# Kernel tuning notes

Hardware: AMD Instinct MI355X
Metric: run time of the kernel (lower is better)

Reference implementation:

```python
import jax, jax.numpy as jnp
import numpy as np

N_SRC, N_DST, E = 50000, 50000, 800000
D_GT, D_AG = 64, 64
HID, HEADS = 256, 4
FPH = HID // HEADS  # 64
N_ACT = 16
NEG_SLOPE = 0.2  # DGL GATv2Conv default negative_slope


def setup_inputs() -> dict:
    key = jax.random.key(0)
    ks = jax.random.split(key, 16)
    f32 = jnp.float32
    return {
        "feat_gt": jax.random.normal(ks[0], (N_SRC, D_GT), f32),
        "feat_agent": jax.random.normal(ks[1], (N_DST, D_AG), f32),
        "h0": jax.random.normal(ks[2], (N_DST, HID), f32),
        "edge_src": jax.random.randint(ks[3], (E,), 0, N_SRC),
        "edge_dst": jax.random.randint(ks[4], (E,), 0, N_DST),
        "W_src": jax.random.normal(ks[5], (D_GT, HID), f32) * 0.1,
        "b_src": jnp.zeros((HID,), f32),
        "W_dst": jax.random.normal(ks[6], (D_AG, HID), f32) * 0.1,
        "b_dst": jnp.zeros((HID,), f32),
        "attn": jax.random.normal(ks[7], (HEADS, FPH), f32) * 0.1,
        "W_res": jax.random.normal(ks[8], (D_AG, HID), f32) * 0.1,
        "b_res": jnp.zeros((HID,), f32),
        "W_ih": jax.random.normal(ks[9], (3 * HID, HID), f32) * 0.05,
        "W_hh": jax.random.normal(ks[10], (3 * HID, HID), f32) * 0.05,
        "b_ih": jnp.zeros((3 * HID,), f32),
        "b_hh": jnp.zeros((3 * HID,), f32),
        "W_out": jax.random.normal(ks[11], (HID, N_ACT), f32) * 0.05,
        "b_out": jnp.zeros((N_ACT,), f32),
    }


def _gatv2(feat_gt, feat_agent, edge_src, edge_dst,
           W_src, b_src, W_dst, b_dst, attn, W_res, b_res):
    # GATv2Conv (bipartite, share_weights=False, residual=True, activation=ReLU)
    fs = (feat_gt @ W_src + b_src).reshape(N_SRC, HEADS, FPH)    # [Ns,H,F]
    fd = (feat_agent @ W_dst + b_dst).reshape(N_DST, HEADS, FPH)  # [Nd,H,F]
    e = fs[edge_src] + fd[edge_dst]                               # [E,H,F]
    e = jnp.where(e > 0, e, NEG_SLOPE * e)                        # LeakyReLU
    score = jnp.einsum('ehf,hf->eh', e, attn)                     # [E,H]
    # edge softmax segmented by destination node
    smax = jax.lax.stop_gradient(
        jax.ops.segment_max(score, edge_dst, num_segments=N_DST))  # [Nd,H]
    ex = jnp.exp(score - smax[edge_dst])
    den = jax.ops.segment_sum(ex, edge_dst, num_segments=N_DST)   # [Nd,H]
    alpha = ex / den[edge_dst]                                    # [E,H]
    msg = alpha[:, :, None] * fs[edge_src]                        # [E,H,F]
    rst = jax.ops.segment_sum(msg, edge_dst, num_segments=N_DST)  # [Nd,H,F]
    rst = rst.reshape(N_DST, HID) + (feat_agent @ W_res + b_res)  # residual
    return jax.nn.relu(rst)


def _gru_cell(x, h, W_ih, W_hh, b_ih, b_hh):
    gi = x @ W_ih.T + b_ih
    gh = h @ W_hh.T + b_hh
    ir, iz, inn = jnp.split(gi, 3, axis=-1)
    hr, hz, hn = jnp.split(gh, 3, axis=-1)
    r = jax.nn.sigmoid(ir + hr)
    z = jax.nn.sigmoid(iz + hz)
    n = jnp.tanh(inn + r * hn)
    return (1.0 - z) * n + z * h


def reference(feat_gt, feat_agent, h0, edge_src, edge_dst,
              W_src, b_src, W_dst, b_dst, attn, W_res, b_res,
              W_ih, W_hh, b_ih, b_hh, W_out, b_out):
    x = _gatv2(feat_gt, feat_agent, edge_src, edge_dst,
               W_src, b_src, W_dst, b_dst, attn, W_res, b_res)  # [Nd,HID]
    h = _gru_cell(x, h0, W_ih, W_hh, b_ih, b_hh)                # [Nd,HID]
    logits = h @ W_out + b_out                                  # [Nd,N_ACT]
    return (logits, h)
```

## Files before the change

kernel.cpp:

```cpp
#include <hip/hip_runtime.h>
#include <stdint.h>

#define N_SRCN 50000
#define N_DSTN 50000
#define NE     800000
#define HIDN   256
#define NEG    0.2f

typedef __attribute__((ext_vector_type(8)))  short short8;
typedef __attribute__((ext_vector_type(16))) float float16v;

__device__ __forceinline__ float bf2f(unsigned short u){
    union { unsigned u32; float f; } c; c.u32 = ((unsigned)u) << 16; return c.f;
}
__device__ __forceinline__ unsigned short f2bf(float f){
    union { float f; unsigned u; } c; c.f = f;
    unsigned r = c.u + 0x7fffu + ((c.u >> 16) & 1u);
    return (unsigned short)(r >> 16);
}
__device__ __forceinline__ float4 ld4b(const unsigned short* p){
    uint2 u = *reinterpret_cast<const uint2*>(p);
    float4 r;
    r.x = bf2f((unsigned short)(u.x & 0xffff));
    r.y = bf2f((unsigned short)(u.x >> 16));
    r.z = bf2f((unsigned short)(u.y & 0xffff));
    r.w = bf2f((unsigned short)(u.y >> 16));
    return r;
}

__global__ void pack_kernel(const float* __restrict__ Wsrc, const float* __restrict__ Wdst,
                            const float* __restrict__ Wres, const float* __restrict__ Wih,
                            const float* __restrict__ Whh,
                            unsigned short* __restrict__ Wt2,
                            unsigned short* __restrict__ Wf){
    int i = blockIdx.x * 256 + threadIdx.x;
    if (i < 49152){
        int which = i >> 14, j = i & 16383;
        int k = j >> 8, c = j & 255;
        const float* W = (which == 0) ? Wsrc : (which == 1 ? Wdst : Wres);
        float v = W[j];
        int off = which * 16384 + (c >> 5) * 2048 + (k >> 4) * 512
                + (((k >> 3) & 1) * 32 + (c & 31)) * 8 + (k & 7);
        Wt2[off] = f2bf(v);
    } else if (i < 49152 + 196608){
        int o = i - 49152;
        int row = o >> 8, k = o & 255;
        int g = row >> 8, c = row & 255;
        float v = Wih[o];
        int off = g * 131072 + (c >> 5) * 16384 + (k >> 4) * 512
                + (((k >> 3) & 1) * 32 + (c & 31)) * 8 + (k & 7);
        Wf[off] = f2bf(v);
    } else if (i < 49152 + 393216){
        int o = i - 49152 - 196608;
        int row = o >> 8, k = o & 255;
        int g = row >> 8, c = row & 255;
        float v = Whh[o];
        int off = g * 131072 + (c >> 5) * 16384 + (16 + (k >> 4)) * 512
                + (((k >> 3) & 1) * 32 + (c & 31)) * 8 + (k & 7);
        Wf[off] = f2bf(v);
    }
}

__global__ void convh_kernel(const float* __restrict__ h, unsigned short* __restrict__ hb){
    int i = blockIdx.x * 256 + threadIdx.x;
    if (i < N_DSTN * 64){
        float4 v = reinterpret_cast<const float4*>(h)[i];
        uint2 o;
        o.x = (unsigned)f2bf(v.x) | ((unsigned)f2bf(v.y) << 16);
        o.y = (unsigned)f2bf(v.z) | ((unsigned)f2bf(v.w) << 16);
        reinterpret_cast<uint2*>(hb)[i] = o;
    }
}

__global__ __launch_bounds__(256) void proj_kernel(
        const float* __restrict__ A, const unsigned short* __restrict__ Wt2,
        const float* __restrict__ bias, unsigned short* __restrict__ out){
    __shared__ unsigned short As[64 * 72];
    __shared__ unsigned short Cs[64 * 72];
    int tid = threadIdx.x;
    int m0 = blockIdx.y * 64;
    #pragma unroll
    for (int i = 0; i < 4; ++i){
        int ci = tid + i * 256;
        int row = ci >> 4;
        int k4 = (ci & 15) << 2;
        int gr = m0 + row; if (gr >= N_SRCN) gr = N_SRCN - 1;
        float4 v = *reinterpret_cast<const float4*>(A + (size_t)gr * 64 + k4);
        unsigned short* dp = As + row * 72 + k4;
        dp[0] = f2bf(v.x); dp[1] = f2bf(v.y); dp[2] = f2bf(v.z); dp[3] = f2bf(v.w);
    }
    __syncthreads();
    int lane = tid & 63, w = tid >> 6;
    int l31 = lane & 31, half = lane >> 5;
    int msub = (w & 1) * 32;
    int cbw = blockIdx.x * 2 + (w >> 1);
    const unsigned short* bb = Wt2 + cbw * 2048 + lane * 8;
    const unsigned short* ap = As + (msub + l31) * 72 + half * 8;
    float16v acc = {0,0,0,0,0,0,0,0,0,0,0,0,0,0,0,0};
    #pragma unroll
    for (int ks = 0; ks < 4; ++ks){
        short8 a = *reinterpret_cast<const short8*>(ap + ks * 16);
        short8 b = *reinterpret_cast<const short8*>(bb + ks * 512);
        acc = __builtin_amdgcn_mfma_f32_32x32x16_bf16(a, b, acc, 0, 0, 0);
    }
    float bv = bias[cbw * 32 + l31];
    int ccol = (w >> 1) * 32 + l31;
    #pragma unroll
    for (int r = 0; r < 16; ++r){
        int row = (r & 3) + 8 * (r >> 2) + 4 * half + msub;
        Cs[row * 72 + ccol] = f2bf(acc[r] + bv);
    }
    __syncthreads();
    int srow = tid >> 2, chunk = tid & 3;
    int gr2 = m0 + srow;
    if (gr2 < N_SRCN){
        const uint4* sp = reinterpret_cast<const uint4*>(Cs + srow * 72 + chunk * 16);
        uint4* gp = reinterpret_cast<uint4*>(out + (size_t)gr2 * 256 + blockIdx.x * 64 + chunk * 16);
        gp[0] = sp[0];
        gp[1] = sp[1];
    }
}

__global__ void degree_kernel(const int* __restrict__ dst, int* __restrict__ deg){
    int i = blockIdx.x * 256 + threadIdx.x;
    if (i < NE) atomicAdd(&deg[dst[i]], 1);
}

__global__ void scan1_kernel(const int* __restrict__ deg, int* __restrict__ bsum){
    __shared__ int s[256];
    int tid = threadIdx.x;
    int i = blockIdx.x * 256 + tid;
    s[tid] = (i < N_DSTN) ? deg[i] : 0;
    __syncthreads();
    #pragma unroll
    for (int off = 128; off; off >>= 1){
        if (tid < off) s[tid] += s[tid + off];
        __syncthreads();
    }
    if (tid == 0) bsum[blockIdx.x] = s[0];
}

__global__ void scan2_kernel(const int* __restrict__ bsum, int* __restrict__ boff){
    __shared__ int s[256];
    int tid = threadIdx.x;
    int v = (tid < 196) ? bsum[tid] : 0;
    s[tid] = v;
    __syncthreads();
    #pragma unroll
    for (int off = 1; off < 256; off <<= 1){
        int t = (tid >= off) ? s[tid - off] : 0;
        __syncthreads();
        s[tid] += t;
        __syncthreads();
    }
    if (tid < 196) boff[tid] = s[tid] - v;
}

__global__ void scan3_kernel(const int* __restrict__ deg, const int* __restrict__ boff,
                             int* __restrict__ ptr, int* __restrict__ cursor){
    __shared__ int s[256];
    int tid = threadIdx.x;
    int i = blockIdx.x * 256 + tid;
    int v = (i < N_DSTN) ? deg[i] : 0;
    s[tid] = v;
    __syncthreads();
    #pragma unroll
    for (int off = 1; off < 256; off <<= 1){
        int t = (tid >= off) ? s[tid - off] : 0;
        __syncthreads();
        s[tid] += t;
        __syncthreads();
    }
    int ex = s[tid] - v + boff[blockIdx.x];
    if (i < N_DSTN){ ptr[i] = ex; cursor[i] = ex; }
}

__global__ void scatter_kernel(const int* __restrict__ src, const int* __restrict__ dst,
                               int* __restrict__ cursor, int* __restrict__ csr){
    int i = blockIdx.x * 256 + threadIdx.x;
    if (i < NE){
        int d = dst[i];
        int pos = atomicAdd(&cursor[d], 1);
        csr[pos] = src[i];
    }
}

__global__ __launch_bounds__(256) void aggregate_kernel(
        const unsigned short* __restrict__ fs, const unsigned short* __restrict__ fd,
        const unsigned short* __restrict__ res, const float* __restrict__ attn,
        const int* __restrict__ ptr, const int* __restrict__ deg,
        const int* __restrict__ csr, unsigned short* __restrict__ x){
    int wv = threadIdx.x >> 6;
    int d = blockIdx.x * 4 + wv;
    if (d >= N_DSTN) return;
    int lane = threadIdx.x & 63;
    int c4 = lane * 4;
    float4 fdv = ld4b(fd + (size_t)d * 256 + c4);
    float4 at = *reinterpret_cast<const float4*>(attn + (lane >> 4) * 64 + (lane & 15) * 4);
    int p = ptr[d], dg = deg[d];
    float l = 0.f;
    float4 acc = make_float4(0.f, 0.f, 0.f, 0.f);
    for (int base = 0; base < dg; base += 64){
        int cnt = min(64, dg - base);
        int sreg = (lane < cnt) ? csr[p + base + lane] : 0;
        float4 b0 = ld4b(fs + (size_t)__shfl(sreg, 0) * 256 + c4);
        float4 b1 = ld4b(fs + (size_t)__shfl(sreg, 1 & 63) * 256 + c4);
        float4 b2 = ld4b(fs + (size_t)__shfl(sreg, 2 & 63) * 256 + c4);
        float4 b3 = ld4b(fs + (size_t)__shfl(sreg, 3 & 63) * 256 + c4);
        for (int j = 0; j < cnt; j += 4){
            float4 n0 = ld4b(fs + (size_t)__shfl(sreg, (j + 4) & 63) * 256 + c4);
            float4 n1 = ld4b(fs + (size_t)__shfl(sreg, (j + 5) & 63) * 256 + c4);
            float4 n2 = ld4b(fs + (size_t)__shfl(sreg, (j + 6) & 63) * 256 + c4);
            float4 n3 = ld4b(fs + (size_t)__shfl(sreg, (j + 7) & 63) * 256 + c4);
#define PROC(BV, T) { \
            float ex = BV.x + fdv.x; ex = ex > 0.f ? ex : NEG * ex; \
            float ey = BV.y + fdv.y; ey = ey > 0.f ? ey : NEG * ey; \
            float ez = BV.z + fdv.z; ez = ez > 0.f ? ez : NEG * ez; \
            float ew = BV.w + fdv.w; ew = ew > 0.f ? ew : NEG * ew; \
            float part = ex * at.x + ey * at.y + ez * at.z + ew * at.w; \
            part += __shfl_xor(part, 1); \
            part += __shfl_xor(part, 2); \
            part += __shfl_xor(part, 4); \
            part += __shfl_xor(part, 8); \
            float wgt = ((j + (T)) < cnt) ? __expf(part) : 0.f; \
            l += wgt; \
            acc.x = fmaf(wgt, BV.x, acc.x); \
            acc.y = fmaf(wgt, BV.y, acc.y); \
            acc.z = fmaf(wgt, BV.z, acc.z); \
            acc.w = fmaf(wgt, BV.w, acc.w); }
            PROC(b0, 0) PROC(b1, 1) PROC(b2, 2) PROC(b3, 3)
#undef PROC
            b0 = n0; b1 = n1; b2 = n2; b3 = n3;
        }
    }
    float inv = (l > 0.f) ? 1.f / l : 0.f;
    float4 rv = ld4b(res + (size_t)d * 256 + c4);
    float xx = fmaxf(fmaf(acc.x, inv, rv.x), 0.f);
    float xy = fmaxf(fmaf(acc.y, inv, rv.y), 0.f);
    float xz = fmaxf(fmaf(acc.z, inv, rv.z), 0.f);
    float xw = fmaxf(fmaf(acc.w, inv, rv.w), 0.f);
    uint2 o;
    o.x = (unsigned)f2bf(xx) | ((unsigned)f2bf(xy) << 16);
    o.y = (unsigned)f2bf(xz) | ((unsigned)f2bf(xw) << 16);
    *reinterpret_cast<uint2*>(x + (size_t)d * 256 + c4) = o;
}

__global__ __launch_bounds__(256, 3) void gru_kernel(
        const unsigned short* __restrict__ Xb, const unsigned short* __restrict__ Hb,
        const float* __restrict__ H0, const unsigned short* __restrict__ Wf,
        const float* __restrict__ bih, const float* __restrict__ bhh,
        float* __restrict__ outH){
    __shared__ unsigned short As[128 * 136];
    int tid = threadIdx.x;
    int m0 = blockIdx.y * 128;
    int w = tid >> 6, lane = tid & 63;
    int l31 = lane & 31, half = lane >> 5;
    int cb = blockIdx.x;
    int cg = cb * 32 + l31;
    const unsigned short* bb = Wf + cb * 16384 + lane * 8;
    float16v ar  = {0,0,0,0,0,0,0,0,0,0,0,0,0,0,0,0};
    float16v az = ar, anx = ar, anh = ar;
    #pragma unroll
    for (int kc = 0; kc < 512; kc += 128){
        const unsigned short* srcb = (kc < 256) ? (Xb + kc) : (Hb + (kc - 256));
        __syncthreads();
        #pragma unroll
        for (int i = 0; i < 8; ++i){
            int ci = tid + i * 256;
            int row = ci >> 4;
            int k8 = (ci & 15) << 3;
            int gr = m0 + row; if (gr >= N_DSTN) gr = N_DSTN - 1;
            *reinterpret_cast<uint4*>(As + row * 136 + k8) =
                *reinterpret_cast<const uint4*>(srcb + (size_t)gr * 256 + k8);
        }
        __syncthreads();
        const unsigned short* ap = As + (w * 32 + l31) * 136 + half * 8;
        #pragma unroll
        for (int ks = 0; ks < 8; ++ks){
            int kk = (kc >> 4) + ks;
            short8 a  = *reinterpret_cast<const short8*>(ap + ks * 16);
            short8 br = *reinterpret_cast<const short8*>(bb + (size_t)kk * 512);
            short8 bz = *reinterpret_cast<const short8*>(bb + 131072 + (size_t)kk * 512);
            short8 bn = *reinterpret_cast<const short8*>(bb + 262144 + (size_t)kk * 512);
            ar = __builtin_amdgcn_mfma_f32_32x32x16_bf16(a, br, ar, 0, 0, 0);
            az = __builtin_amdgcn_mfma_f32_32x32x16_bf16(a, bz, az, 0, 0, 0);
            if (kc < 256) anx = __builtin_amdgcn_mfma_f32_32x32x16_bf16(a, bn, anx, 0, 0, 0);
            else          anh = __builtin_amdgcn_mfma_f32_32x32x16_bf16(a, bn, anh, 0, 0, 0);
        }
    }
    float rb = bih[cg] + bhh[cg];
    float zb = bih[256 + cg] + bhh[256 + cg];
    float bin = bih[512 + cg], bhn = bhh[512 + cg];
    #pragma unroll
    for (int r = 0; r < 16; ++r){
        int m = m0 + w * 32 + (r & 3) + 8 * (r >> 2) + 4 * half;
        if (m < N_DSTN){
            float h0v = H0[(size_t)m * 256 + cg];
            float rr = 1.f / (1.f + __expf(-(ar[r] + rb)));
            float zz = 1.f / (1.f + __expf(-(az[r] + zb)));
            float nx = anx[r] + bin + rr * (anh[r] + bhn);
            float tm = __expf(-2.f * fabsf(nx));
            float nn = (1.f - tm) / (1.f + tm);
            nn = (nx >= 0.f) ? nn : -nn;
            outH[(size_t)m * 256 + cg] = (1.f - zz) * nn + zz * h0v;
        }
    }
}

__global__ __launch_bounds__(256) void logits_kernel(
        const float* __restrict__ H, const float* __restrict__ Wout,
        const float* __restrict__ bout, float* __restrict__ outL){
    __shared__ float Hl[16 * 260];
    __shared__ float Wl[16 * 260];
    int tid = threadIdx.x;
    int m0 = blockIdx.x * 16;
    #pragma unroll
    for (int i = 0; i < 4; ++i){
        int ci = tid + i * 256;
        int row = ci >> 6;
        int c4 = (ci & 63) << 2;
        int gr = m0 + row; if (gr >= N_DSTN) gr = N_DSTN - 1;
        float4 v = *reinterpret_cast<const float4*>(H + (size_t)gr * 256 + c4);
        float* dp = Hl + row * 260 + c4;
        dp[0] = v.x; dp[1] = v.y; dp[2] = v.z; dp[3] = v.w;
    }
    #pragma unroll
    for (int i = 0; i < 16; ++i){
        int ci = tid + i * 256;
        int c = ci >> 4, j = ci & 15;
        Wl[j * 260 + c] = Wout[c * 16 + j];
    }
    __syncthreads();
    int row = tid >> 4, j = tid & 15;
    const float* hr = Hl + row * 260;
    const float* wr = Wl + j * 260;
    float acc = bout[j];
    #pragma unroll
    for (int c = 0; c < 256; c += 4){
        float4 hv = *reinterpret_cast<const float4*>(hr + c);
        float4 wv = *reinterpret_cast<const float4*>(wr + c);
        acc = fmaf(hv.x, wv.x, fmaf(hv.y, wv.y, fmaf(hv.z, wv.z, fmaf(hv.w, wv.w, acc))));
    }
    int m = m0 + row;
    if (m < N_DSTN) outL[m * 16 + j] = acc;
}

extern "C" void kernel_launch(void* const* d_in, const int* in_sizes, int n_in,
                              void* d_out, int out_size, void* d_ws, size_t ws_size,
                              hipStream_t stream){
    const float* feat_gt = (const float*)d_in[0];
    const float* feat_ag = (const float*)d_in[1];
    const float* h0      = (const float*)d_in[2];
    const int*   e_src   = (const int*)d_in[3];
    const int*   e_dst   = (const int*)d_in[4];
    const float* W_src   = (const float*)d_in[5];
    const float* b_src   = (const float*)d_in[6];
    const float* W_dst   = (const float*)d_in[7];
    const float* b_dst   = (const float*)d_in[8];
    const float* attn    = (const float*)d_in[9];
    const float* W_res   = (const float*)d_in[10];
    const float* b_res   = (const float*)d_in[11];
    const float* W_ih    = (const float*)d_in[12];
    const float* W_hh    = (const float*)d_in[13];
    const float* b_ih    = (const float*)d_in[14];
    const float* b_hh    = (const float*)d_in[15];
    const float* W_out   = (const float*)d_in[16];
    const float* b_out   = (const float*)d_in[17];

    float* outL = (float*)d_out;
    float* outH = outL + (size_t)N_DSTN * 16;

    char* ws = (char*)d_ws;
    size_t off = 0;
    auto alloc = [&](size_t bytes) -> void* {
        void* p = ws + off; off = (off + bytes + 255) & ~(size_t)255; return p;
    };
    unsigned short* fs   = (unsigned short*)alloc((size_t)N_SRCN * 256 * 2);
    unsigned short* fd   = (unsigned short*)alloc((size_t)N_DSTN * 256 * 2);
    unsigned short* res  = (unsigned short*)alloc((size_t)N_DSTN * 256 * 2);
    unsigned short* xb   = (unsigned short*)alloc((size_t)N_DSTN * 256 * 2);
    unsigned short* hb   = (unsigned short*)alloc((size_t)N_DSTN * 256 * 2);
    unsigned short* Wt2  = (unsigned short*)alloc(49152 * 2);
    unsigned short* Wf   = (unsigned short*)alloc(393216 * 2);
    int* deg    = (int*)alloc(N_DSTN * 4);
    int* ptr    = (int*)alloc(N_DSTN * 4);
    int* cursor = (int*)alloc(N_DSTN * 4);
    int* csr    = (int*)alloc((size_t)NE * 4);
    int* bsum   = (int*)alloc(256 * 4);
    int* boff   = (int*)alloc(256 * 4);

    hipMemsetAsync(deg, 0, N_DSTN * 4, stream);
    pack_kernel<<<1728, 256, 0, stream>>>(W_src, W_dst, W_res, W_ih, W_hh, Wt2, Wf);
    convh_kernel<<<12500, 256, 0, stream>>>(h0, hb);

    dim3 pg(4, 782);
    proj_kernel<<<pg, 256, 0, stream>>>(feat_gt, Wt2, b_src, fs);
    proj_kernel<<<pg, 256, 0, stream>>>(feat_ag, Wt2 + 16384, b_dst, fd);
    proj_kernel<<<pg, 256, 0, stream>>>(feat_ag, Wt2 + 32768, b_res, res);

    degree_kernel<<<3125, 256, 0, stream>>>(e_dst, deg);
    scan1_kernel<<<196, 256, 0, stream>>>(deg, bsum);
    scan2_kernel<<<1, 256, 0, stream>>>(bsum, boff);
    scan3_kernel<<<196, 256, 0, stream>>>(deg, boff, ptr, cursor);
    scatter_kernel<<<3125, 256, 0, stream>>>(e_src, e_dst, cursor, csr);
    aggregate_kernel<<<12500, 256, 0, stream>>>(fs, fd, res, attn, ptr, deg, csr, xb);

    gru_kernel<<<dim3(8, 391), 256, 0, stream>>>(xb, hb, h0, Wf, b_ih, b_hh, outH);
    logits_kernel<<<3125, 256, 0, stream>>>(outH, W_out, b_out, outL);
}
```

Before: 497.1 us.

## Fuse h0 bf16 conversion into GRU, merge projection launches, XCD-aware GRU mapping

Removes the separate h0-to-bf16 conversion kernel and its buffer: the GRU kernel now loads fp32 h0 directly and converts it while staging into shared memory. The three projection GEMM launches are merged into one launch using blockIdx.z to select input, weights, bias and output. The GRU grid is flattened and remapped so the 8 column blocks of a row strip land on the same XCD, aiming for L2 reuse of the activation rows, and the occupancy hint is raised from 3 to 4. The tradeoff is that each GRU block now reads fp32 h0, twice the bytes of bf16, for every column block, and the higher occupancy hint may constrain registers.

After: 485.2 us. 2.4% less time.

```diff
diff --git a/kernel.cpp b/kernel.cpp
--- a/kernel.cpp
+++ b/kernel.cpp
@@ -61,22 +61,20 @@
     }
 }
 
-__global__ void convh_kernel(const float* __restrict__ h, unsigned short* __restrict__ hb){
-    int i = blockIdx.x * 256 + threadIdx.x;
-    if (i < N_DSTN * 64){
-        float4 v = reinterpret_cast<const float4*>(h)[i];
-        uint2 o;
-        o.x = (unsigned)f2bf(v.x) | ((unsigned)f2bf(v.y) << 16);
-        o.y = (unsigned)f2bf(v.z) | ((unsigned)f2bf(v.w) << 16);
-        reinterpret_cast<uint2*>(hb)[i] = o;
-    }
-}
-
 __global__ __launch_bounds__(256) void proj_kernel(
-        const float* __restrict__ A, const unsigned short* __restrict__ Wt2,
-        const float* __restrict__ bias, unsigned short* __restrict__ out){
+        const float* __restrict__ Agt, const float* __restrict__ Aag,
+        const unsigned short* __restrict__ Wt2,
+        const float* __restrict__ bsrc, const float* __restrict__ bdst,
+        const float* __restrict__ bres,
+        unsigned short* __restrict__ fs, unsigned short* __restrict__ fd,
+        unsigned short* __restrict__ resb){
     __shared__ unsigned short As[64 * 72];
     __shared__ unsigned short Cs[64 * 72];
+    int z = blockIdx.z;
+    const float* A = (z == 0) ? Agt : Aag;
+    const float* bias = (z == 0) ? bsrc : (z == 1 ? bdst : bres);
+    unsigned short* out = (z == 0) ? fs : (z == 1 ? fd : resb);
+    const unsigned short* Wb = Wt2 + z * 16384;
     int tid = threadIdx.x;
     int m0 = blockIdx.y * 64;
     #pragma unroll
@@ -94,7 +92,7 @@
     int l31 = lane & 31, half = lane >> 5;
     int msub = (w & 1) * 32;
     int cbw = blockIdx.x * 2 + (w >> 1);
-    const unsigned short* bb = Wt2 + cbw * 2048 + lane * 8;
+    const unsigned short* bb = Wb + cbw * 2048 + lane * 8;
     const unsigned short* ap = As + (msub + l31) * 72 + half * 8;
     float16v acc = {0,0,0,0,0,0,0,0,0,0,0,0,0,0,0,0};
     #pragma unroll
@@ -245,33 +243,54 @@
     *reinterpret_cast<uint2*>(x + (size_t)d * 256 + c4) = o;
 }
 
-__global__ __launch_bounds__(256, 3) void gru_kernel(
-        const unsigned short* __restrict__ Xb, const unsigned short* __restrict__ Hb,
+__global__ __launch_bounds__(256, 4) void gru_kernel(
+        const unsigned short* __restrict__ Xb,
         const float* __restrict__ H0, const unsigned short* __restrict__ Wf,
         const float* __restrict__ bih, const float* __restrict__ bhh,
         float* __restrict__ outH){
     __shared__ unsigned short As[128 * 136];
     int tid = threadIdx.x;
-    int m0 = blockIdx.y * 128;
+    int sid = blockIdx.x;
+    int xcd = sid & 7, rr_ = sid >> 3;
+    int strip = xcd * 49 + (rr_ >> 3);
+    int cb = rr_ & 7;
+    int m0 = strip << 7;
     int w = tid >> 6, lane = tid & 63;
     int l31 = lane & 31, half = lane >> 5;
-    int cb = blockIdx.x;
     int cg = cb * 32 + l31;
     const unsigned short* bb = Wf + cb * 16384 + lane * 8;
     float16v ar  = {0,0,0,0,0,0,0,0,0,0,0,0,0,0,0,0};
     float16v az = ar, anx = ar, anh = ar;
     #pragma unroll
     for (int kc = 0; kc < 512; kc += 128){
-        const unsigned short* srcb = (kc < 256) ? (Xb + kc) : (Hb + (kc - 256));
-        __syncthreads();
-        #pragma unroll
-        for (int i = 0; i < 8; ++i){
-            int ci = tid + i * 256;
-            int row = ci >> 4;
-            int k8 = (ci & 15) << 3;
-            int gr = m0 + row; if (gr >= N_DSTN) gr = N_DSTN - 1;
-            *reinterpret_cast<uint4*>(As + row * 136 + k8) =
-                *reinterpret_cast<const uint4*>(srcb + (size_t)gr * 256 + k8);
+        __syncthreads();
+        if (kc < 256){
+            #pragma unroll
+            for (int i = 0; i < 8; ++i){
+                int ci = tid + i * 256;
+                int row = ci >> 4;
+                int k8 = (ci & 15) << 3;
+                int gr = m0 + row; if (gr >= N_DSTN) gr = N_DSTN - 1;
+                *reinterpret_cast<uint4*>(As + row * 136 + k8) =
+                    *reinterpret_cast<const uint4*>(Xb + (size_t)gr * 256 + kc + k8);
+            }
+        } else {
+            #pragma unroll
+            for (int i = 0; i < 8; ++i){
+                int ci = tid + i * 256;
+                int row = ci >> 4;
+                int k8 = (ci & 15) << 3;
+                int gr = m0 + row; if (gr >= N_DSTN) gr = N_DSTN - 1;
+                const float* hp = H0 + (size_t)gr * 256 + (kc - 256) + k8;
+                float4 f0 = *reinterpret_cast<const float4*>(hp);
+                float4 f1 = *reinterpret_cast<const float4*>(hp + 4);
+                uint4 o;
+                o.x = (unsigned)f2bf(f0.x) | ((unsigned)f2bf(f0.y) << 16);
+                o.y = (unsigned)f2bf(f0.z) | ((unsigned)f2bf(f0.w) << 16);
+                o.z = (unsigned)f2bf(f1.x) | ((unsigned)f2bf(f1.y) << 16);
+                o.w = (unsigned)f2bf(f1.z) | ((unsigned)f2bf(f1.w) << 16);
+                *reinterpret_cast<uint4*>(As + row * 136 + k8) = o;
+            }
         }
         __syncthreads();
         const unsigned short* ap = As + (w * 32 + l31) * 136 + half * 8;
@@ -296,9 +315,9 @@
         int m = m0 + w * 32 + (r & 3) + 8 * (r >> 2) + 4 * half;
         if (m < N_DSTN){
             float h0v = H0[(size_t)m * 256 + cg];
-            float rr = 1.f / (1.f + __expf(-(ar[r] + rb)));
+            float rrg = 1.f / (1.f + __expf(-(ar[r] + rb)));
             float zz = 1.f / (1.f + __expf(-(az[r] + zb)));
-            float nx = anx[r] + bin + rr * (anh[r] + bhn);
+            float nx = anx[r] + bin + rrg * (anh[r] + bhn);
             float tm = __expf(-2.f * fabsf(nx));
             float nn = (1.f - tm) / (1.f + tm);
             nn = (nx >= 0.f) ? nn : -nn;
@@ -379,7 +398,6 @@
     unsigned short* fd   = (unsigned short*)alloc((size_t)N_DSTN * 256 * 2);
     unsigned short* res  = (unsigned short*)alloc((size_t)N_DSTN * 256 * 2);
     unsigned short* xb   = (unsigned short*)alloc((size_t)N_DSTN * 256 * 2);
-    unsigned short* hb   = (unsigned short*)alloc((size_t)N_DSTN * 256 * 2);
     unsigned short* Wt2  = (unsigned short*)alloc(49152 * 2);
     unsigned short* Wf   = (unsigned short*)alloc(393216 * 2);
     int* deg    = (int*)alloc(N_DSTN * 4);
@@ -391,12 +409,9 @@
 
     hipMemsetAsync(deg, 0, N_DSTN * 4, stream);
     pack_kernel<<<1728, 256, 0, stream>>>(W_src, W_dst, W_res, W_ih, W_hh, Wt2, Wf);
-    convh_kernel<<<12500, 256, 0, stream>>>(h0, hb);
-
-    dim3 pg(4, 782);
-    proj_kernel<<<pg, 256, 0, stream>>>(feat_gt, Wt2, b_src, fs);
-    proj_kernel<<<pg, 256, 0, stream>>>(feat_ag, Wt2 + 16384, b_dst, fd);
-    proj_kernel<<<pg, 256, 0, stream>>>(feat_ag, Wt2 + 32768, b_res, res);
+
+    proj_kernel<<<dim3(4, 782, 3), 256, 0, stream>>>(feat_gt, feat_ag, Wt2,
+                                                     b_src, b_dst, b_res, fs, fd, res);
 
     degree_kernel<<<3125, 256, 0, stream>>>(e_dst, deg);
     scan1_kernel<<<196, 256, 0, stream>>>(deg, bsum);
@@ -405,6 +420,6 @@
     scatter_kernel<<<3125, 256, 0, stream>>>(e_src, e_dst, cursor, csr);
     aggregate_kernel<<<12500, 256, 0, stream>>>(fs, fd, res, attn, ptr, deg, csr, xb);
 
-    gru_kernel<<<dim3(8, 391), 256, 0, stream>>>(xb, hb, h0, Wf, b_ih, b_hh, outH);
+    gru_kernel<<<3136, 256, 0, stream>>>(xb, h0, Wf, b_ih, b_hh, outH);
     logits_kernel<<<3125, 256, 0, stream>>>(outH, W_out, b_out, outL);
 }
```
